# Kernel tuning notes

Measured on AMD Instinct MI355X. Metric: run time of the kernel, lower is better.

The kernel has to match this reference:

```python
import jax, jax.numpy as jnp
import numpy as np

D = 128
N_DRUG = 100000
N_PROT = 50000
E_DD, E_DP, E_PD = 800000, 600000, 600000
EPS = 1e-5


def setup_inputs() -> dict:
    key = jax.random.key(0)
    ks = jax.random.split(key, 19)
    f32 = jnp.float32
    return {
        "x_drug": jax.random.normal(ks[0], (N_DRUG, D), f32),
        "x_prot": jax.random.normal(ks[1], (N_PROT, D), f32),
        "Wagg_dd": jax.random.normal(ks[2], (D, D), f32) * 0.05,
        "Wagg_dp": jax.random.normal(ks[3], (D, D), f32) * 0.05,
        "Wagg_pd": jax.random.normal(ks[4], (D, D), f32) * 0.05,
        "W_drug": jax.random.normal(ks[5], (D, 2 * D), f32) * 0.05,
        "b_drug": jax.random.normal(ks[6], (D,), f32) * 0.01,
        "W_prot": jax.random.normal(ks[7], (D, 2 * D), f32) * 0.05,
        "b_prot": jax.random.normal(ks[8], (D,), f32) * 0.01,
        "g_drug": jnp.ones((D,), f32),
        "be_drug": jnp.zeros((D,), f32),
        "g_prot": jnp.ones((D,), f32),
        "be_prot": jnp.zeros((D,), f32),
        "ei_dd_src": jax.random.randint(ks[9], (E_DD,), 0, N_DRUG, jnp.int64 if jax.config.jax_enable_x64 else jnp.int32),
        "ei_dd_dst": jax.random.randint(ks[10], (E_DD,), 0, N_DRUG),
        "ei_dp_src": jax.random.randint(ks[11], (E_DP,), 0, N_DRUG),
        "ei_dp_dst": jax.random.randint(ks[12], (E_DP,), 0, N_PROT),
        "ei_pd_src": jax.random.randint(ks[13], (E_PD,), 0, N_PROT),
        "ei_pd_dst": jax.random.randint(ks[14], (E_PD,), 0, N_DRUG),
    }


def _rel_agg(x_src, W_agg, src_idx, dst_idx, n_dst):
    # gather -> per-relation Linear (no bias) + ReLU -> scatter-mean
    h = jax.nn.relu(x_src[src_idx] @ W_agg.T)            # [E, D]
    s = jax.ops.segment_sum(h, dst_idx, num_segments=n_dst)
    c = jax.ops.segment_sum(jnp.ones((src_idx.shape[0],), h.dtype), dst_idx, num_segments=n_dst)
    return s / jnp.maximum(c, 1.0)[:, None]


def _layernorm(x, g, b):
    mu = jnp.mean(x, axis=-1, keepdims=True)
    var = jnp.mean(jnp.square(x - mu), axis=-1, keepdims=True)
    return (x - mu) * jax.lax.rsqrt(var + EPS) * g + b


def _node_update(h_self, h_agg, W, b, g, be):
    h = jax.nn.relu(jnp.concatenate([h_self, h_agg], axis=-1) @ W.T + b)
    return _layernorm(h + h_self, g, be)  # dropout is identity in eval


def reference(x_drug, x_prot, Wagg_dd, Wagg_dp, Wagg_pd, W_drug, b_drug,
              W_prot, b_prot, g_drug, be_drug, g_prot, be_prot,
              ei_dd_src, ei_dd_dst, ei_dp_src, ei_dp_dst, ei_pd_src, ei_pd_dst):
    agg_dd = _rel_agg(x_drug, Wagg_dd, ei_dd_src, ei_dd_dst, N_DRUG)
    agg_pd = _rel_agg(x_prot, Wagg_pd, ei_pd_src, ei_pd_dst, N_DRUG)
    agg_drug = (agg_dd + agg_pd) * 0.5                   # mean over relations into 'drug'
    agg_prot = _rel_agg(x_drug, Wagg_dp, ei_dp_src, ei_dp_dst, N_PROT)
    out_drug = _node_update(x_drug, agg_drug, W_drug, b_drug, g_drug, be_drug)
    out_prot = _node_update(x_prot, agg_prot, W_prot, b_prot, g_prot, be_prot)
    # pack the per-type outputs into one array [N_DRUG + N_PROT, D]
    return jnp.concatenate([out_drug, out_prot], axis=0)
```

## Files before the change

kernel.cpp:

```cpp
#include <hip/hip_runtime.h>

#define D 128
#define ND 100000
#define NP 50000
#define NE_DD 800000
#define NE_DP 600000
#define NE_PD 600000
#define NE_TOT 2000000

#define NTOT 250000
#define NBC 490
#define NC 250880
#define CHUNKA 4096
#define NBLKA 489
#define CHUNKIT 16
#define SEGCAP 8192

#define TF_BD 782
#define TF_BP 196
#define NU_BD 391
#define NU_BP 196

typedef __bf16 bf16;
typedef __attribute__((ext_vector_type(8))) __bf16 bf16x8;
typedef __attribute__((ext_vector_type(2))) __bf16 bf16x2;
typedef __attribute__((ext_vector_type(4))) float f32x4;
typedef __attribute__((ext_vector_type(2))) float f32x2;

#define OFF_WDD   0UL
#define OFF_WDP   32768UL
#define OFF_WPD   65536UL
#define OFF_WDRUG 98304UL
#define OFF_WPROT 163840UL
#define OFF_YDD   229376UL
#define OFF_YDP   (OFF_YDD + 25600000UL)
#define OFF_YPD   (OFF_YDP + 25600000UL)
#define OFF_AGGD  (OFF_YPD + 12800000UL)
#define OFF_AGGP  (OFF_AGGD + 25600000UL)
#define OFF_BCNT  (OFF_AGGP + 12800000UL)
#define OFF_GCUR  (OFF_BCNT + 2048UL)
#define OFF_CBASE (OFF_GCUR + 2048UL)
#define OFF_RP    (OFF_CBASE + 2048UL)
#define OFF_PAIRS (OFF_RP + 1003520UL)
#define OFF_POOL  (OFF_PAIRS + 16000000UL)

__device__ __forceinline__ unsigned enc1(float f)
{
    unsigned t = __float_as_uint(f * 0x1p-120f);
    t = (t + 0x80000u) >> 20;
    return t > 0x7Eu ? 0x7Eu : t;
}
__device__ __forceinline__ unsigned enc4(float a, float b, float c, float d)
{
    return enc1(a) | (enc1(b) << 8) | (enc1(c) << 16) | (enc1(d) << 24);
}

__global__ __launch_bounds__(256) void prep_kernel(
    const float* __restrict__ w0, const float* __restrict__ w1,
    const float* __restrict__ w2, const float* __restrict__ w3,
    const float* __restrict__ w4,
    bf16* __restrict__ o0, bf16* __restrict__ o1, bf16* __restrict__ o2,
    bf16* __restrict__ o3, bf16* __restrict__ o4,
    const int* __restrict__ dd_dst, const int* __restrict__ pd_dst,
    const int* __restrict__ dp_dst, int* __restrict__ bcnt)
{
    int m = blockIdx.y;
    int t = threadIdx.x;
    if (m == 5) {
        __shared__ int h[NBC];
        for (int i = t; i < NBC; i += 256) h[i] = 0;
        __syncthreads();
        for (int e = blockIdx.x * 256 + t; e < NE_TOT; e += 128 * 256) {
            int didx;
            if (e < NE_DD) didx = dd_dst[e];
            else if (e < NE_DD + NE_PD) didx = ND + pd_dst[e - NE_DD];
            else didx = 2 * ND + dp_dst[e - NE_DD - NE_PD];
            atomicAdd(&h[didx >> 9], 1);
        }
        __syncthreads();
        for (int i = t; i < NBC; i += 256)
            if (h[i]) atomicAdd(&bcnt[i], h[i]);
        return;
    }
    int i = blockIdx.x * 256 + t;
    const float* src; bf16* dst; int n; bool perm;
    switch (m) {
        case 0: src = w0; dst = o0; n = D * D; perm = false; break;
        case 1: src = w1; dst = o1; n = D * D; perm = false; break;
        case 2: src = w2; dst = o2; n = D * D; perm = false; break;
        case 3: src = w3; dst = o3; n = D * 2 * D; perm = true; break;
        default: src = w4; dst = o4; n = D * 2 * D; perm = true; break;
    }
    if (i < n) {
        int si = i;
        if (perm) {
            int col = i & 255;
            if (col >= 128) {
                int p = col - 128;
                si = (i & ~255) | (128 + (p & 7) * 16 + (p >> 3));
            }
        }
        dst[i] = (bf16)src[si];
    }
}

__global__ __launch_bounds__(256) void scan_kernel(
    const int* __restrict__ bcnt, int* __restrict__ cbase, int* __restrict__ gcur)
{
    __shared__ int ps[256];
    int t = threadIdx.x;
    int i0 = 2 * t, i1 = 2 * t + 1;
    int c0 = (i0 < NBC) ? bcnt[i0] : 0;
    int c1 = (i1 < NBC) ? bcnt[i1] : 0;
    ps[t] = c0 + c1;
    __syncthreads();
#pragma unroll
    for (int off = 1; off < 256; off <<= 1) {
        int add = (t >= off) ? ps[t - off] : 0;
        __syncthreads();
        ps[t] += add;
        __syncthreads();
    }
    int excl = ps[t] - (c0 + c1);
    if (i0 <= NBC) cbase[i0] = excl;
    if (i0 < NBC) gcur[i0] = excl;
    if (i1 < NBC) { cbase[i1] = excl + c0; gcur[i1] = excl + c0; }
}

__device__ __forceinline__ bf16x8 load_a_f32(const float* __restrict__ xr)
{
    float4 f0 = *(const float4*)xr;
    float4 f1 = *(const float4*)(xr + 4);
    bf16x8 a;
    a[0] = (bf16)f0.x; a[1] = (bf16)f0.y; a[2] = (bf16)f0.z; a[3] = (bf16)f0.w;
    a[4] = (bf16)f1.x; a[5] = (bf16)f1.y; a[6] = (bf16)f1.z; a[7] = (bf16)f1.w;
    return a;
}

__device__ __forceinline__ void transform_drug(
    const float* __restrict__ x, const bf16* __restrict__ W1,
    const bf16* __restrict__ W2, unsigned char* __restrict__ y1,
    unsigned char* __restrict__ y2, int blk)
{
    int lane = threadIdx.x & 63;
    int wave = threadIdx.x >> 6;
    int q = lane >> 4, c = lane & 15;
    int mb = blk * 128 + wave * 32;

    f32x4 acc1[2][8], acc2[2][8];
#pragma unroll
    for (int mt = 0; mt < 2; mt++)
#pragma unroll
        for (int nt = 0; nt < 8; nt++) { acc1[mt][nt] = 0; acc2[mt][nt] = 0; }

#pragma unroll
    for (int kb = 0; kb < 4; kb++) {
        int k = kb * 32 + q * 8;
        bf16x8 a[2];
#pragma unroll
        for (int mt = 0; mt < 2; mt++) {
            int row = min(mb + mt * 16 + c, ND - 1);
            a[mt] = load_a_f32(x + (long)row * D + k);
        }
#pragma unroll
        for (int nt = 0; nt < 8; nt++) {
            bf16x8 b1 = *(const bf16x8*)(W1 + (nt * 16 + c) * D + k);
            bf16x8 b2 = *(const bf16x8*)(W2 + (nt * 16 + c) * D + k);
#pragma unroll
            for (int mt = 0; mt < 2; mt++) {
                acc1[mt][nt] = __builtin_amdgcn_mfma_f32_16x16x32_bf16(a[mt], b1, acc1[mt][nt], 0, 0, 0);
                acc2[mt][nt] = __builtin_amdgcn_mfma_f32_16x16x32_bf16(a[mt], b2, acc2[mt][nt], 0, 0, 0);
            }
        }
    }
#pragma unroll
    for (int mt = 0; mt < 2; mt++)
#pragma unroll
        for (int r = 0; r < 4; r++) {
            int row = mb + mt * 16 + q * 4 + r;
            if (row < ND) {
                float v1[8], v2[8];
#pragma unroll
                for (int nt = 0; nt < 8; nt++) {
                    v1[nt] = fmaxf(acc1[mt][nt][r], 0.f);
                    v2[nt] = fmaxf(acc2[mt][nt][r], 0.f);
                }
                uint2 p1, p2;
                p1.x = enc4(v1[0], v1[1], v1[2], v1[3]);
                p1.y = enc4(v1[4], v1[5], v1[6], v1[7]);
                p2.x = enc4(v2[0], v2[1], v2[2], v2[3]);
                p2.y = enc4(v2[4], v2[5], v2[6], v2[7]);
                *(uint2*)(y1 + (long)row * D + c * 8) = p1;
                *(uint2*)(y2 + (long)row * D + c * 8) = p2;
            }
        }
}

__device__ __forceinline__ void transform_prot(
    const float* __restrict__ x, const bf16* __restrict__ W1,
    unsigned char* __restrict__ y1, int blk)
{
    int lane = threadIdx.x & 63;
    int wave = threadIdx.x >> 6;
    int q = lane >> 4, c = lane & 15;
    int mb = blk * 256 + wave * 64;

    f32x4 acc[4][8];
#pragma unroll
    for (int mt = 0; mt < 4; mt++)
#pragma unroll
        for (int nt = 0; nt < 8; nt++) acc[mt][nt] = 0;

#pragma unroll
    for (int kb = 0; kb < 4; kb++) {
        int k = kb * 32 + q * 8;
        bf16x8 a[4];
#pragma unroll
        for (int mt = 0; mt < 4; mt++) {
            int row = min(mb + mt * 16 + c, NP - 1);
            a[mt] = load_a_f32(x + (long)row * D + k);
        }
#pragma unroll
        for (int nt = 0; nt < 8; nt++) {
            bf16x8 b1 = *(const bf16x8*)(W1 + (nt * 16 + c) * D + k);
#pragma unroll
            for (int mt = 0; mt < 4; mt++)
                acc[mt][nt] = __builtin_amdgcn_mfma_f32_16x16x32_bf16(a[mt], b1, acc[mt][nt], 0, 0, 0);
        }
    }
#pragma unroll
    for (int mt = 0; mt < 4; mt++)
#pragma unroll
        for (int r = 0; r < 4; r++) {
            int row = mb + mt * 16 + q * 4 + r;
            if (row < NP) {
                float v[8];
#pragma unroll
                for (int nt = 0; nt < 8; nt++)
                    v[nt] = fmaxf(acc[mt][nt][r], 0.f);
                uint2 p1;
                p1.x = enc4(v[0], v[1], v[2], v[3]);
                p1.y = enc4(v[4], v[5], v[6], v[7]);
                *(uint2*)(y1 + (long)row * D + c * 8) = p1;
            }
        }
}

__global__ __launch_bounds__(256, 2) void transform_kernel(
    const float* __restrict__ x_drug, const float* __restrict__ x_prot,
    const bf16* __restrict__ Wdd, const bf16* __restrict__ Wdp,
    const bf16* __restrict__ Wpd,
    unsigned char* __restrict__ y_dd, unsigned char* __restrict__ y_dp,
    unsigned char* __restrict__ y_pd)
{
    int blk = blockIdx.x;
    if (blk < TF_BD)
        transform_drug(x_drug, Wdd, Wdp, y_dd, y_dp, blk);
    else
        transform_prot(x_prot, Wpd, y_pd, blk - TF_BD);
}

__global__ __launch_bounds__(256) void binA_kernel(
    const int* __restrict__ dd_src, const int* __restrict__ dd_dst,
    const int* __restrict__ pd_src, const int* __restrict__ pd_dst,
    const int* __restrict__ dp_src, const int* __restrict__ dp_dst,
    int* __restrict__ gcur, unsigned* __restrict__ pairs)
{
    __shared__ int h[NBC];
    __shared__ int gb[NBC];
    __shared__ int2 pr[CHUNKA];
    __shared__ unsigned short rk[CHUNKA];
    for (int i = threadIdx.x; i < NBC; i += 256) h[i] = 0;
    __syncthreads();
    int base = blockIdx.x * CHUNKA;
    for (int it = 0; it < CHUNKIT; it++) {
        int idx = it * 256 + threadIdx.x;
        int e = base + idx;
        int didx = -1, sv = 0;
        if (e < NE_TOT) {
            if (e < NE_DD) { didx = dd_dst[e]; sv = dd_src[e]; }
            else if (e < NE_DD + NE_PD) { int u = e - NE_DD; didx = ND + pd_dst[u]; sv = pd_src[u]; }
            else { int u = e - NE_DD - NE_PD; didx = 2 * ND + dp_dst[u]; sv = dp_src[u]; }
            rk[idx] = (unsigned short)atomicAdd(&h[didx >> 9], 1);
        }
        pr[idx] = make_int2(didx, sv);
    }
    __syncthreads();
    for (int b = threadIdx.x; b < NBC; b += 256) {
        int c = h[b];
        gb[b] = c ? atomicAdd(&gcur[b], c) : 0;
    }
    __syncthreads();
    for (int it = 0; it < CHUNKIT; it++) {
        int idx = it * 256 + threadIdx.x;
        int2 p = pr[idx];
        if (p.x >= 0)
            pairs[gb[p.x >> 9] + rk[idx]] =
                ((unsigned)(p.x & 511) << 17) | (unsigned)p.y;
    }
}

__global__ __launch_bounds__(256) void sortB_kernel(
    const int* __restrict__ cbase, const unsigned* __restrict__ pairs,
    int* __restrict__ pool, int* __restrict__ rp)
{
    __shared__ int h[512];
    __shared__ int excl[512];
    __shared__ int ps[256];
    __shared__ unsigned short rk[SEGCAP];
    __shared__ int outl[SEGCAP];

    int b = blockIdx.x;
    int s0 = cbase[b], s1 = cbase[b + 1];
    int n = s1 - s0;
    if (n > SEGCAP) n = SEGCAP;
    int t = threadIdx.x;
    h[t] = 0; h[t + 256] = 0;
    __syncthreads();

    for (int i = t; i < n; i += 256) {
        unsigned p = pairs[s0 + i];
        rk[i] = (unsigned short)atomicAdd(&h[p >> 17], 1);
    }
    __syncthreads();

    int c0 = h[2 * t], c1 = h[2 * t + 1];
    ps[t] = c0 + c1;
    __syncthreads();
#pragma unroll
    for (int off = 1; off < 256; off <<= 1) {
        int add = (t >= off) ? ps[t - off] : 0;
        __syncthreads();
        ps[t] += add;
        __syncthreads();
    }
    int pe = ps[t] - (c0 + c1);
    excl[2 * t] = pe;
    excl[2 * t + 1] = pe + c0;
    __syncthreads();

    int nb = b * 512;
    rp[nb + 2 * t] = s0 + excl[2 * t];
    rp[nb + 2 * t + 1] = s0 + excl[2 * t + 1];

    for (int i = t; i < n; i += 256) {
        unsigned p = pairs[s0 + i];
        outl[excl[p >> 17] + rk[i]] = (int)(p & 0x1FFFFu);
    }
    __syncthreads();
    for (int i = t; i < n; i += 256)
        pool[s0 + i] = outl[i];
}

__device__ __forceinline__ void accw(unsigned short w, f32x2* acc)
{
    float lo = __uint_as_float((unsigned)(w & 0xFFu) << 20);
    float hi = __uint_as_float((unsigned)(w >> 8) << 20);
    acc->x = fmaf(lo, 0x1p120f, acc->x);
    acc->y = fmaf(hi, 0x1p120f, acc->y);
}

__device__ __forceinline__ void acc_seg(
    const int* __restrict__ pool, int s, int e,
    const unsigned short* __restrict__ y, int lane, f32x2* acc)
{
    int j = s;
    for (; j + 8 <= e; j += 8) {
        unsigned short u[8];
#pragma unroll
        for (int t = 0; t < 8; t++)
            u[t] = y[(long)pool[j + t] * 64 + lane];
#pragma unroll
        for (int t = 0; t < 8; t++) accw(u[t], acc);
    }
    if (j + 4 <= e) {
        unsigned short u[4];
#pragma unroll
        for (int t = 0; t < 4; t++)
            u[t] = y[(long)pool[j + t] * 64 + lane];
#pragma unroll
        for (int t = 0; t < 4; t++) accw(u[t], acc);
        j += 4;
    }
    if (j + 2 <= e) {
        unsigned short u0 = y[(long)pool[j] * 64 + lane];
        unsigned short u1 = y[(long)pool[j + 1] * 64 + lane];
        accw(u0, acc); accw(u1, acc);
        j += 2;
    }
    if (j < e)
        accw(y[(long)pool[j] * 64 + lane], acc);
}

__global__ __launch_bounds__(256) void gather_kernel(
    const int* __restrict__ rp, const int* __restrict__ pool,
    const unsigned short* __restrict__ y_dd,
    const unsigned short* __restrict__ y_pd,
    const unsigned short* __restrict__ y_dp,
    bf16* __restrict__ agg_d, bf16* __restrict__ agg_p)
{
    int wid = blockIdx.x * 4 + (threadIdx.x >> 6);
    int lane = threadIdx.x & 63;

    if (wid < ND) {
        int g = wid;
        int s1 = rp[g], e1 = rp[g + 1];
        int s2 = rp[ND + g], e2 = rp[ND + g + 1];
        f32x2 a; a.x = 0.f; a.y = 0.f;
        f32x2 b; b.x = 0.f; b.y = 0.f;
        acc_seg(pool, s1, e1, y_dd, lane, &a);
        acc_seg(pool, s2, e2, y_pd, lane, &b);
        float i1 = 0.5f / (float)max(e1 - s1, 1);
        float i2 = 0.5f / (float)max(e2 - s2, 1);
        f32x2 r = a * i1 + b * i2;
        bf16x2 o; o[0] = (bf16)r.x; o[1] = (bf16)r.y;
        *(bf16x2*)(agg_d + (long)g * D + lane * 2) = o;
    } else if (wid < ND + NP) {
        int p = wid - ND;
        int s1 = rp[2 * ND + p], e1 = rp[2 * ND + p + 1];
        f32x2 a; a.x = 0.f; a.y = 0.f;
        acc_seg(pool, s1, e1, y_dp, lane, &a);
        float i1 = 1.0f / (float)max(e1 - s1, 1);
        f32x2 r = a * i1;
        bf16x2 o; o[0] = (bf16)r.x; o[1] = (bf16)r.y;
        *(bf16x2*)(agg_p + (long)p * D + lane * 2) = o;
    }
}

__device__ __forceinline__ void node_update_body(
    const float* __restrict__ x, const bf16* __restrict__ agg,
    const bf16* __restrict__ W, const float* __restrict__ b,
    const float* __restrict__ g, const float* __restrict__ be,
    float* __restrict__ out, int M, int blk)
{
    int lane = threadIdx.x & 63;
    int wave = threadIdx.x >> 6;
    int q = lane >> 4, c = lane & 15;
    int mb = blk * 256 + wave * 64;

    f32x4 acc[4][8];
#pragma unroll
    for (int mt = 0; mt < 4; mt++)
#pragma unroll
        for (int nt = 0; nt < 8; nt++) acc[mt][nt] = 0;

#pragma unroll
    for (int kb = 0; kb < 8; kb++) {
        bf16x8 a[4];
#pragma unroll
        for (int mt = 0; mt < 4; mt++) {
            int row = min(mb + mt * 16 + c, M - 1);
            if (kb < 4)
                a[mt] = load_a_f32(x + (long)row * D + kb * 32 + q * 8);
            else
                a[mt] = *(const bf16x8*)(agg + (long)row * D + (kb - 4) * 32 + q * 8);
        }
#pragma unroll
        for (int nt = 0; nt < 8; nt++) {
            bf16x8 bw = *(const bf16x8*)(W + (nt * 16 + c) * (2 * D) + kb * 32 + q * 8);
#pragma unroll
            for (int mt = 0; mt < 4; mt++)
                acc[mt][nt] = __builtin_amdgcn_mfma_f32_16x16x32_bf16(a[mt], bw, acc[mt][nt], 0, 0, 0);
        }
    }

    float bv[8], gv[8], bev[8];
#pragma unroll
    for (int nt = 0; nt < 8; nt++) {
        int col = nt * 16 + c;
        bv[nt] = b[col]; gv[nt] = g[col]; bev[nt] = be[col];
    }
#pragma unroll
    for (int mt = 0; mt < 4; mt++)
#pragma unroll
        for (int r = 0; r < 4; r++) {
            int row = mb + mt * 16 + q * 4 + r;
            int rowc = min(row, M - 1);
            const float* xr = x + (long)rowc * D + c;
            float v[8];
            float sum = 0.f, sq = 0.f;
#pragma unroll
            for (int nt = 0; nt < 8; nt++) {
                float h = fmaxf(acc[mt][nt][r] + bv[nt], 0.f);
                float t = h + xr[nt * 16];
                v[nt] = t; sum += t; sq += t * t;
            }
#pragma unroll
            for (int m = 1; m < 16; m <<= 1) {
                sum += __shfl_xor(sum, m, 64);
                sq  += __shfl_xor(sq,  m, 64);
            }
            float mu   = sum * (1.f / 128.f);
            float var  = sq  * (1.f / 128.f) - mu * mu;
            float rstd = rsqrtf(var + 1e-5f);
            if (row < M) {
                float* op = out + (long)row * D + c;
#pragma unroll
                for (int nt = 0; nt < 8; nt++)
                    op[nt * 16] = (v[nt] - mu) * rstd * gv[nt] + bev[nt];
            }
        }
}

__global__ __launch_bounds__(256, 2) void node_update_kernel(
    const float* __restrict__ x_drug, const float* __restrict__ x_prot,
    const bf16* __restrict__ agg_d, const bf16* __restrict__ agg_p,
    const bf16* __restrict__ Wdrug, const float* __restrict__ b_drug,
    const float* __restrict__ g_drug, const float* __restrict__ be_drug,
    const bf16* __restrict__ Wprot, const float* __restrict__ b_prot,
    const float* __restrict__ g_prot, const float* __restrict__ be_prot,
    float* __restrict__ out)
{
    int blk = blockIdx.x;
    if (blk < NU_BD)
        node_update_body(x_drug, agg_d, Wdrug, b_drug, g_drug, be_drug,
                         out, ND, blk);
    else
        node_update_body(x_prot, agg_p, Wprot, b_prot, g_prot, be_prot,
                         out + (long)ND * D, NP, blk - NU_BD);
}

extern "C" void kernel_launch(void* const* d_in, const int* in_sizes, int n_in,
                              void* d_out, int out_size, void* d_ws, size_t ws_size,
                              hipStream_t stream)
{
    const float* x_drug  = (const float*)d_in[0];
    const float* x_prot  = (const float*)d_in[1];
    const float* Wagg_dd = (const float*)d_in[2];
    const float* Wagg_dp = (const float*)d_in[3];
    const float* Wagg_pd = (const float*)d_in[4];
    const float* W_drug  = (const float*)d_in[5];
    const float* b_drug  = (const float*)d_in[6];
    const float* W_prot  = (const float*)d_in[7];
    const float* b_prot  = (const float*)d_in[8];
    const float* g_drug  = (const float*)d_in[9];
    const float* be_drug = (const float*)d_in[10];
    const float* g_prot  = (const float*)d_in[11];
    const float* be_prot = (const float*)d_in[12];
    const int* dd_src = (const int*)d_in[13];
    const int* dd_dst = (const int*)d_in[14];
    const int* dp_src = (const int*)d_in[15];
    const int* dp_dst = (const int*)d_in[16];
    const int* pd_src = (const int*)d_in[17];
    const int* pd_dst = (const int*)d_in[18];

    char* ws = (char*)d_ws;
    bf16* Wdd   = (bf16*)(ws + OFF_WDD);
    bf16* Wdp   = (bf16*)(ws + OFF_WDP);
    bf16* Wpd   = (bf16*)(ws + OFF_WPD);
    bf16* Wdrug = (bf16*)(ws + OFF_WDRUG);
    bf16* Wprot = (bf16*)(ws + OFF_WPROT);
    unsigned char* y_dd = (unsigned char*)(ws + OFF_YDD);
    unsigned char* y_dp = (unsigned char*)(ws + OFF_YDP);
    unsigned char* y_pd = (unsigned char*)(ws + OFF_YPD);
    bf16* agg_d = (bf16*)(ws + OFF_AGGD);
    bf16* agg_p = (bf16*)(ws + OFF_AGGP);
    int* bcnt   = (int*)(ws + OFF_BCNT);
    int* gcur   = (int*)(ws + OFF_GCUR);
    int* cbase  = (int*)(ws + OFF_CBASE);
    int* rp     = (int*)(ws + OFF_RP);
    unsigned* pairs = (unsigned*)(ws + OFF_PAIRS);
    int* pool   = (int*)(ws + OFF_POOL);
    float* out  = (float*)d_out;

    hipMemsetAsync(bcnt, 0, NBC * sizeof(int), stream);

    prep_kernel<<<dim3(128, 6), 256, 0, stream>>>(
        Wagg_dd, Wagg_dp, Wagg_pd, W_drug, W_prot,
        Wdd, Wdp, Wpd, Wdrug, Wprot,
        dd_dst, pd_dst, dp_dst, bcnt);

    scan_kernel<<<1, 256, 0, stream>>>(bcnt, cbase, gcur);

    binA_kernel<<<NBLKA, 256, 0, stream>>>(
        dd_src, dd_dst, pd_src, pd_dst, dp_src, dp_dst, gcur, pairs);

    sortB_kernel<<<NBC, 256, 0, stream>>>(cbase, pairs, pool, rp);

    transform_kernel<<<TF_BD + TF_BP, 256, 0, stream>>>(
        x_drug, x_prot, Wdd, Wdp, Wpd, y_dd, y_dp, y_pd);

    gather_kernel<<<(ND + NP + 3) / 4, 256, 0, stream>>>(
        rp, pool, (const unsigned short*)y_dd, (const unsigned short*)y_pd,
        (const unsigned short*)y_dp, agg_d, agg_p);

    node_update_kernel<<<NU_BD + NU_BP, 256, 0, stream>>>(
        x_drug, x_prot, agg_d, agg_p,
        Wdrug, b_drug, g_drug, be_drug,
        Wprot, b_prot, g_prot, be_prot, out);
}
```

Measured before the change: 415.4 us.

## Split histogram into wide kernel, drop memset, interleave dual-relation gather loads

The destination histogram moves out of prep_kernel, where it ran on only 128 blocks, into its own hist_kernel with one block per 4096-edge chunk. The bucket counters are now zeroed inside prep_kernel, which removes the separate memset. The transform kernel is launched before the histogram, scan and sort stages. The drug gather now loads four dd and four pd rows before accumulating them, to keep more memory requests in flight. This adds one kernel launch and makes the gather loop more complex.

```diff
diff --git a/kernel.cpp b/kernel.cpp
--- a/kernel.cpp
+++ b/kernel.cpp
@@ -61,28 +61,14 @@
     const float* __restrict__ w4,
     bf16* __restrict__ o0, bf16* __restrict__ o1, bf16* __restrict__ o2,
     bf16* __restrict__ o3, bf16* __restrict__ o4,
-    const int* __restrict__ dd_dst, const int* __restrict__ pd_dst,
-    const int* __restrict__ dp_dst, int* __restrict__ bcnt)
+    int* __restrict__ bcnt)
 {
     int m = blockIdx.y;
-    int t = threadIdx.x;
+    int i = blockIdx.x * 256 + threadIdx.x;
     if (m == 5) {
-        __shared__ int h[NBC];
-        for (int i = t; i < NBC; i += 256) h[i] = 0;
-        __syncthreads();
-        for (int e = blockIdx.x * 256 + t; e < NE_TOT; e += 128 * 256) {
-            int didx;
-            if (e < NE_DD) didx = dd_dst[e];
-            else if (e < NE_DD + NE_PD) didx = ND + pd_dst[e - NE_DD];
-            else didx = 2 * ND + dp_dst[e - NE_DD - NE_PD];
-            atomicAdd(&h[didx >> 9], 1);
-        }
-        __syncthreads();
-        for (int i = t; i < NBC; i += 256)
-            if (h[i]) atomicAdd(&bcnt[i], h[i]);
+        if (i < NBC) bcnt[i] = 0;
         return;
     }
-    int i = blockIdx.x * 256 + t;
     const float* src; bf16* dst; int n; bool perm;
     switch (m) {
         case 0: src = w0; dst = o0; n = D * D; perm = false; break;
@@ -102,29 +88,6 @@
         }
         dst[i] = (bf16)src[si];
     }
-}
-
-__global__ __launch_bounds__(256) void scan_kernel(
-    const int* __restrict__ bcnt, int* __restrict__ cbase, int* __restrict__ gcur)
-{
-    __shared__ int ps[256];
-    int t = threadIdx.x;
-    int i0 = 2 * t, i1 = 2 * t + 1;
-    int c0 = (i0 < NBC) ? bcnt[i0] : 0;
-    int c1 = (i1 < NBC) ? bcnt[i1] : 0;
-    ps[t] = c0 + c1;
-    __syncthreads();
-#pragma unroll
-    for (int off = 1; off < 256; off <<= 1) {
-        int add = (t >= off) ? ps[t - off] : 0;
-        __syncthreads();
-        ps[t] += add;
-        __syncthreads();
-    }
-    int excl = ps[t] - (c0 + c1);
-    if (i0 <= NBC) cbase[i0] = excl;
-    if (i0 < NBC) gcur[i0] = excl;
-    if (i1 < NBC) { cbase[i1] = excl + c0; gcur[i1] = excl + c0; }
 }
 
 __device__ __forceinline__ bf16x8 load_a_f32(const float* __restrict__ xr)
@@ -260,6 +223,52 @@
         transform_prot(x_prot, Wpd, y_pd, blk - TF_BD);
 }
 
+__global__ __launch_bounds__(256) void hist_kernel(
+    const int* __restrict__ dd_dst, const int* __restrict__ pd_dst,
+    const int* __restrict__ dp_dst, int* __restrict__ bcnt)
+{
+    __shared__ int h[NBC];
+    for (int i = threadIdx.x; i < NBC; i += 256) h[i] = 0;
+    __syncthreads();
+    int base = blockIdx.x * CHUNKA;
+    for (int it = 0; it < CHUNKIT; it++) {
+        int e = base + it * 256 + threadIdx.x;
+        if (e < NE_TOT) {
+            int didx;
+            if (e < NE_DD) didx = dd_dst[e];
+            else if (e < NE_DD + NE_PD) didx = ND + pd_dst[e - NE_DD];
+            else didx = 2 * ND + dp_dst[e - NE_DD - NE_PD];
+            atomicAdd(&h[didx >> 9], 1);
+        }
+    }
+    __syncthreads();
+    for (int i = threadIdx.x; i < NBC; i += 256)
+        if (h[i]) atomicAdd(&bcnt[i], h[i]);
+}
+
+__global__ __launch_bounds__(256) void scan_kernel(
+    const int* __restrict__ bcnt, int* __restrict__ cbase, int* __restrict__ gcur)
+{
+    __shared__ int ps[256];
+    int t = threadIdx.x;
+    int i0 = 2 * t, i1 = 2 * t + 1;
+    int c0 = (i0 < NBC) ? bcnt[i0] : 0;
+    int c1 = (i1 < NBC) ? bcnt[i1] : 0;
+    ps[t] = c0 + c1;
+    __syncthreads();
+#pragma unroll
+    for (int off = 1; off < 256; off <<= 1) {
+        int add = (t >= off) ? ps[t - off] : 0;
+        __syncthreads();
+        ps[t] += add;
+        __syncthreads();
+    }
+    int excl = ps[t] - (c0 + c1);
+    if (i0 <= NBC) cbase[i0] = excl;
+    if (i0 < NBC) gcur[i0] = excl;
+    if (i1 < NBC) { cbase[i1] = excl + c0; gcur[i1] = excl + c0; }
+}
+
 __global__ __launch_bounds__(256) void binA_kernel(
     const int* __restrict__ dd_src, const int* __restrict__ dd_dst,
     const int* __restrict__ pd_src, const int* __restrict__ pd_dst,
@@ -408,8 +417,23 @@
         int s2 = rp[ND + g], e2 = rp[ND + g + 1];
         f32x2 a; a.x = 0.f; a.y = 0.f;
         f32x2 b; b.x = 0.f; b.y = 0.f;
-        acc_seg(pool, s1, e1, y_dd, lane, &a);
-        acc_seg(pool, s2, e2, y_pd, lane, &b);
+        int j1 = s1, j2 = s2;
+        while (j1 + 4 <= e1 && j2 + 4 <= e2) {
+            unsigned short ua[4], ub[4];
+#pragma unroll
+            for (int t = 0; t < 4; t++)
+                ua[t] = y_dd[(long)pool[j1 + t] * 64 + lane];
+#pragma unroll
+            for (int t = 0; t < 4; t++)
+                ub[t] = y_pd[(long)pool[j2 + t] * 64 + lane];
+#pragma unroll
+            for (int t = 0; t < 4; t++) accw(ua[t], &a);
+#pragma unroll
+            for (int t = 0; t < 4; t++) accw(ub[t], &b);
+            j1 += 4; j2 += 4;
+        }
+        acc_seg(pool, j1, e1, y_dd, lane, &a);
+        acc_seg(pool, j2, e2, y_pd, lane, &b);
         float i1 = 0.5f / (float)max(e1 - s1, 1);
         float i2 = 0.5f / (float)max(e2 - s2, 1);
         f32x2 r = a * i1 + b * i2;
@@ -563,22 +587,18 @@
     int* pool   = (int*)(ws + OFF_POOL);
     float* out  = (float*)d_out;
 
-    hipMemsetAsync(bcnt, 0, NBC * sizeof(int), stream);
-
     prep_kernel<<<dim3(128, 6), 256, 0, stream>>>(
         Wagg_dd, Wagg_dp, Wagg_pd, W_drug, W_prot,
-        Wdd, Wdp, Wpd, Wdrug, Wprot,
-        dd_dst, pd_dst, dp_dst, bcnt);
-
+        Wdd, Wdp, Wpd, Wdrug, Wprot, bcnt);
+
+    transform_kernel<<<TF_BD + TF_BP, 256, 0, stream>>>(
+        x_drug, x_prot, Wdd, Wdp, Wpd, y_dd, y_dp, y_pd);
+
+    hist_kernel<<<NBLKA, 256, 0, stream>>>(dd_dst, pd_dst, dp_dst, bcnt);
     scan_kernel<<<1, 256, 0, stream>>>(bcnt, cbase, gcur);
-
     binA_kernel<<<NBLKA, 256, 0, stream>>>(
         dd_src, dd_dst, pd_src, pd_dst, dp_src, dp_dst, gcur, pairs);
-
     sortB_kernel<<<NBC, 256, 0, stream>>>(cbase, pairs, pool, rp);
-
-    transform_kernel<<<TF_BD + TF_BP, 256, 0, stream>>>(
-        x_drug, x_prot, Wdd, Wdp, Wpd, y_dd, y_dp, y_pd);
 
     gather_kernel<<<(ND + NP + 3) / 4, 256, 0, stream>>>(
         rp, pool, (const unsigned short*)y_dd, (const unsigned short*)y_pd,
```

After: 395.2 us. 1.05x faster.
